# Performance work log

Hardware: AMD Instinct MI355X
Metric: run time of the kernel (lower is better)

## Reference

```python
import jax, jax.numpy as jnp
import numpy as np

N_NODES = 50000
N_EDGES = 1000000
HID = 64
L = 3
EPS_MSG = 1e-7   # GENConv message eps
EPS_SM = 1e-16   # PyG scatter-softmax denominator eps
LN_EPS = 1e-5


def layernorm(x, g, b):
    mu = jnp.mean(x, axis=-1, keepdims=True)
    var = jnp.var(x, axis=-1, keepdims=True)
    return (x - mu) * jax.lax.rsqrt(var + LN_EPS) * g + b


def genconv(x, src, dst, edge_attr, t, W1, b1, g1, be1, W2, b2):
    # message: relu(x_j + e_ij) + eps  -> [E, HID]
    msg = jax.nn.relu(x[src] + edge_attr) + EPS_MSG
    # softmax aggregation over incoming edges of each dst node
    logits = msg * t
    m = jax.ops.segment_max(logits, dst, num_segments=N_NODES)
    m = jnp.where(jnp.isfinite(m), m, 0.0)
    e = jnp.exp(logits - m[dst])
    s = jax.ops.segment_sum(e, dst, num_segments=N_NODES) + EPS_SM
    agg = jax.ops.segment_sum((e / s[dst]) * msg, dst, num_segments=N_NODES)
    # root residual + MLP [64 -> 128 -> 64]
    h = agg + x
    h = h @ W1 + b1
    h = jax.nn.relu(layernorm(h, g1, be1))
    return h @ W2 + b2


def setup_inputs() -> dict:
    key = jax.random.key(0)
    ks = jax.random.split(key, 10)
    inp = {
        'x': jax.random.normal(ks[0], (N_NODES, 16), jnp.float32),
        'edge_attr': jax.random.uniform(ks[1], (N_EDGES, 1), jnp.float32),
        'edge_index': jax.random.randint(ks[2], (2, N_EDGES), 0, N_NODES, jnp.int32),
        'W_node': jax.random.normal(ks[3], (16, HID), jnp.float32) / np.sqrt(16.0),
        'b_node': jnp.zeros((HID,), jnp.float32),
        'W_edge': jax.random.normal(ks[4], (1, HID), jnp.float32),
        'b_edge': jnp.zeros((HID,), jnp.float32),
        't': jnp.ones((L,), jnp.float32),
        'W1': jax.random.normal(ks[5], (L, HID, 2 * HID), jnp.float32) / np.sqrt(float(HID)),
        'b1': jnp.zeros((L, 2 * HID), jnp.float32),
        'ln_g': jnp.ones((L, 2 * HID), jnp.float32),
        'ln_b': jnp.zeros((L, 2 * HID), jnp.float32),
        'W2': jax.random.normal(ks[6], (L, 2 * HID, HID), jnp.float32) / np.sqrt(2.0 * HID),
        'b2': jnp.zeros((L, HID), jnp.float32),
        'norm_g': jnp.ones((L, HID), jnp.float32),
        'norm_b': jnp.zeros((L, HID), jnp.float32),
        'W_lin': jax.random.normal(ks[7], (HID, 64), jnp.float32) / np.sqrt(float(HID)),
        'b_lin': jnp.zeros((64,), jnp.float32),
    }
    return inp


def reference(x, edge_attr, edge_index, W_node, b_node, W_edge, b_edge, t,
              W1, b1, ln_g, ln_b, W2, b2, norm_g, norm_b, W_lin, b_lin):
    src, dst = edge_index[0], edge_index[1]
    h = x @ W_node + b_node                 # [N, HID]
    ea = edge_attr @ W_edge + b_edge        # [E, HID]
    # layer 0: conv only
    h = genconv(h, src, dst, ea, t[0], W1[0], b1[0], ln_g[0], ln_b[0], W2[0], b2[0])
    # layers 1..L-1: res+ blocks (norm -> relu -> conv -> residual); dropout is identity in eval
    for i in range(1, L):
        z = jax.nn.relu(layernorm(h, norm_g[i], norm_b[i]))
        h = h + genconv(z, src, dst, ea, t[i], W1[i], b1[i], ln_g[i], ln_b[i], W2[i], b2[i])
    # final norm/act reuses layer 0's norm
    h = jax.nn.relu(layernorm(h, norm_g[0], norm_b[0]))
    # adaptive avg/max pool (N, 64) -> (1, 32): pool over all nodes, channel bins of 2
    avg = h.mean(axis=0).reshape(32, 2).mean(axis=1)
    mx = h.max(axis=0).reshape(32, 2).max(axis=1)
    emb = jnp.concatenate([avg, mx])[None, :]   # [1, 64]
    return emb @ W_lin + b_lin                  # [1, 64]
```

## Files before the change

kernel.cpp:

```cpp
#include <hip/hip_runtime.h>
#include <math.h>

#define N_NODES 50000
#define N_EDGES 1000000
#define HID 64
#define SCAN_NB ((N_NODES + 1 + 255) / 256)
#define N_TILES (N_NODES / 16)
#define NB_F ((N_TILES + 3) / 4)
#define NB2 64
#define VB_S 72
#define UB_S 136
static_assert(N_NODES % 16 == 0, "tile math");
static_assert(N_NODES <= 65536, "src must fit in 16 bits");

typedef __attribute__((ext_vector_type(8))) short short8;
typedef __attribute__((ext_vector_type(4))) float f32x4;

__device__ __forceinline__ unsigned short f2bf(float x) {
    unsigned u = __float_as_uint(x);
    u += 0x7FFFu + ((u >> 16) & 1u);
    return (unsigned short)(u >> 16);
}
__device__ __forceinline__ float bfbits_hi(unsigned pk) {
    return __uint_as_float(pk & 0xFFFF0000u);
}
__device__ __forceinline__ float bf2f(unsigned short v) {
    return __uint_as_float(((unsigned)v) << 16);
}
__device__ __forceinline__ unsigned addpk(unsigned a, unsigned b) {
    float lo = __uint_as_float(a << 16) + __uint_as_float(b << 16);
    float hi = __uint_as_float(a & 0xFFFF0000u) + __uint_as_float(b & 0xFFFF0000u);
    return (unsigned)f2bf(lo) | ((unsigned)f2bf(hi) << 16);
}

__global__ __launch_bounds__(256) void k_node_encode(
    const float* __restrict__ x, const float* __restrict__ Wn,
    const float* __restrict__ bn, unsigned short* __restrict__ zb) {
    int n = blockIdx.x * 4 + (threadIdx.x >> 6);
    int c = threadIdx.x & 63;
    if (n >= N_NODES) return;
    float acc = bn[c];
    const float* xr = x + n * 16;
    #pragma unroll
    for (int k = 0; k < 16; ++k) acc = fmaf(xr[k], Wn[k * 64 + c], acc);
    zb[n * 64 + c] = f2bf(acc);
}

__global__ __launch_bounds__(256) void k_wprep(
    const float* __restrict__ W1, const float* __restrict__ W2,
    unsigned short* __restrict__ w1p, unsigned short* __restrict__ w2p) {
    int i = blockIdx.x * 256 + threadIdx.x;
    if (i >= 3 * 8192) return;
    int L = i >> 13, r = i & 8191;
    int j = r & 7, lane = (r >> 3) & 63;
    int quad = lane >> 4, col = lane & 15;
    {
        int st = r >> 9;
        int s = st >> 3, t = st & 7;
        w1p[i] = f2bf(W1[L * 8192 + (s * 32 + quad * 8 + j) * 128 + t * 16 + col]);
    }
    {
        int ft = r >> 9;
        int s = ft >> 2, t = ft & 3;
        w2p[i] = f2bf(W2[L * 8192 + (s * 32 + quad * 8 + j) * 64 + t * 16 + col]);
    }
}

__global__ __launch_bounds__(256) void k_hist_rank(const int* __restrict__ ei,
                                                   int* __restrict__ cnt, int* __restrict__ rank) {
    int i = blockIdx.x * blockDim.x + threadIdx.x;
    if (i >= N_EDGES) return;
    rank[i] = atomicAdd(&cnt[ei[N_EDGES + i]], 1);
}

__global__ __launch_bounds__(256) void k_scan1(const int* __restrict__ cnt,
                                               int* __restrict__ inc, int* __restrict__ bsum) {
    __shared__ int sh[256];
    int gi = blockIdx.x * 256 + threadIdx.x;
    int v = (gi < N_NODES + 1) ? cnt[gi] : 0;
    sh[threadIdx.x] = v;
    __syncthreads();
    #pragma unroll
    for (int d = 1; d < 256; d <<= 1) {
        int t = (threadIdx.x >= d) ? sh[threadIdx.x - d] : 0;
        __syncthreads();
        sh[threadIdx.x] += t;
        __syncthreads();
    }
    if (gi < N_NODES + 1) inc[gi] = sh[threadIdx.x];
    if (threadIdx.x == 255) bsum[blockIdx.x] = sh[255];
}

__global__ __launch_bounds__(256) void k_scan2(int* __restrict__ bsum) {
    __shared__ int sh[256];
    int t = threadIdx.x;
    sh[t] = (t < SCAN_NB) ? bsum[t] : 0;
    __syncthreads();
    #pragma unroll
    for (int d = 1; d < 256; d <<= 1) {
        int v = (t >= d) ? sh[t - d] : 0;
        __syncthreads();
        sh[t] += v;
        __syncthreads();
    }
    if (t < SCAN_NB) bsum[t] = (t == 0) ? 0 : sh[t - 1];
}

__global__ __launch_bounds__(256) void k_scan3(const int* __restrict__ inc,
                                               const int* __restrict__ cnt,
                                               const int* __restrict__ bsum,
                                               int* __restrict__ offs) {
    int gi = blockIdx.x * 256 + threadIdx.x;
    if (gi < N_NODES + 1) offs[gi] = bsum[blockIdx.x] + inc[gi] - cnt[gi];
}

__global__ __launch_bounds__(256) void k_scatter(
    const int* __restrict__ ei, const float* __restrict__ eattr,
    const int* __restrict__ offs, const int* __restrict__ rank,
    unsigned int* __restrict__ s_pack) {
    int i = blockIdx.x * blockDim.x + threadIdx.x;
    if (i >= N_EDGES) return;
    int d = ei[N_EDGES + i];
    int p = offs[d] + rank[i];
    unsigned pk = ((unsigned)f2bf(eattr[i]) << 16) | (unsigned)(ei[i] & 0xFFFF);
    s_pack[p] = pk;
}

__global__ __launch_bounds__(256) void k_agg(
    const unsigned short* __restrict__ zb, const int* __restrict__ offs,
    const unsigned int* __restrict__ s_pack,
    const float* __restrict__ We, const float* __restrict__ be,
    const float* __restrict__ t, int layer, unsigned short* __restrict__ aggb) {
    int wid = (blockIdx.x * blockDim.x + threadIdx.x) >> 6;
    int lane = threadIdx.x & 63;
    if (wid >= N_NODES) return;
    int beg = offs[wid], end = offs[wid + 1];
    float we = We[lane], bev = be[lane];
    float tl = t[layer];
    float s = 0.f, num = 0.f;
    int i = beg;
    for (; i + 7 < end; i += 8) {
        unsigned pk[8];
        #pragma unroll
        for (int j = 0; j < 8; ++j) pk[j] = s_pack[i + j];
        float zv[8];
        #pragma unroll
        for (int j = 0; j < 8; ++j) zv[j] = bf2f(zb[(pk[j] & 0xFFFFu) * 64 + lane]);
        float acc_s = 0.f, acc_n = 0.f;
        #pragma unroll
        for (int j = 0; j < 8; ++j) {
            float msg = fmaxf(zv[j] + fmaf(bfbits_hi(pk[j]), we, bev), 0.f) + 1e-7f;
            float p = __expf(msg * tl);
            acc_s += p;
            acc_n = fmaf(p, msg, acc_n);
        }
        s += acc_s;
        num += acc_n;
    }
    for (; i < end; ++i) {
        unsigned pk = s_pack[i];
        float zz = bf2f(zb[(pk & 0xFFFFu) * 64 + lane]);
        float msg = fmaxf(zz + fmaf(bfbits_hi(pk), we, bev), 0.f) + 1e-7f;
        float p = __expf(msg * tl);
        s += p;
        num = fmaf(p, msg, num);
    }
    aggb[wid * 64 + lane] = f2bf(num / (s + 1e-16f));
}

__global__ __launch_bounds__(256) void k_mlp(
    const unsigned short* __restrict__ aggb, unsigned short* __restrict__ zb,
    unsigned short* __restrict__ hb,
    const unsigned short* __restrict__ w1p, const unsigned short* __restrict__ w2p,
    const float* __restrict__ b1,
    const float* __restrict__ g1, const float* __restrict__ be1,
    const float* __restrict__ b2,
    const float* __restrict__ ng, const float* __restrict__ nb, int mode,
    float* __restrict__ pb_sum, float* __restrict__ pb_max) {
    __shared__ unsigned short vbuf[4][16 * VB_S];
    __shared__ unsigned short ubuf[4][16 * UB_S];
    __shared__ float lssum[4][4][16], lsmax[4][4][16];
    int lane = threadIdx.x & 63;
    int wave = threadIdx.x >> 6;
    int col = lane & 15, quad = lane >> 4;
    unsigned short* vb = vbuf[wave];
    unsigned short* ub = ubuf[wave];

    short8 w1f[2][8];
    #pragma unroll
    for (int s = 0; s < 2; ++s)
        #pragma unroll
        for (int t = 0; t < 8; ++t)
            w1f[s][t] = *(const short8*)&w1p[(((s * 8 + t) * 64) + lane) * 8];
    short8 w2f[4][4];
    #pragma unroll
    for (int s = 0; s < 4; ++s)
        #pragma unroll
        for (int t = 0; t < 4; ++t)
            w2f[s][t] = *(const short8*)&w2p[(((s * 4 + t) * 64) + lane) * 8];

    float b1f[8], g1f[8], e1f[8];
    #pragma unroll
    for (int t = 0; t < 8; ++t) {
        int ch = t * 16 + col;
        b1f[t] = b1[ch]; g1f[t] = g1[ch]; e1f[t] = be1[ch];
    }
    float b2f_[4], ngf[4], nbf[4];
    #pragma unroll
    for (int t = 0; t < 4; ++t) {
        b2f_[t] = b2[t * 16 + col];
        ngf[t] = ng[t * 16 + col];
        nbf[t] = nb[t * 16 + col];
    }

    float psum[4] = {0.f, 0.f, 0.f, 0.f};
    float pmax[4] = {0.f, 0.f, 0.f, 0.f};
    int nd = lane >> 2;
    int cg = (lane & 3) * 16;
    int tile = blockIdx.x * 4 + wave;

    if (tile < N_TILES) {
        int n0 = tile * 16;
        const uint4* ap = (const uint4*)(aggb + (size_t)(n0 + nd) * 64 + cg);
        const uint4* zp = (const uint4*)(zb + (size_t)(n0 + nd) * 64 + cg);
        uint4 a0 = ap[0], a1 = ap[1], z0 = zp[0], z1 = zp[1];
        uint4 r0, r1;
        r0.x = addpk(a0.x, z0.x); r0.y = addpk(a0.y, z0.y);
        r0.z = addpk(a0.z, z0.z); r0.w = addpk(a0.w, z0.w);
        r1.x = addpk(a1.x, z1.x); r1.y = addpk(a1.y, z1.y);
        r1.z = addpk(a1.z, z1.z); r1.w = addpk(a1.w, z1.w);
        uint4* vdst = (uint4*)&vb[nd * VB_S + cg];
        vdst[0] = r0;
        vdst[1] = r1;

        short8 af0 = *(const short8*)&vb[col * VB_S + quad * 8];
        short8 af1 = *(const short8*)&vb[col * VB_S + 32 + quad * 8];
        f32x4 au[8];
        #pragma unroll
        for (int t = 0; t < 8; ++t) {
            f32x4 c = {0.f, 0.f, 0.f, 0.f};
            c = __builtin_amdgcn_mfma_f32_16x16x32_bf16(af0, w1f[0][t], c, 0, 0, 0);
            c = __builtin_amdgcn_mfma_f32_16x16x32_bf16(af1, w1f[1][t], c, 0, 0, 0);
            au[t] = c;
        }
        #pragma unroll
        for (int r = 0; r < 4; ++r) {
            float sx = 0.f, sq = 0.f;
            #pragma unroll
            for (int t = 0; t < 8; ++t) {
                float v = au[t][r] + b1f[t];
                sx += v; sq += v * v;
            }
            #pragma unroll
            for (int mask = 1; mask < 16; mask <<= 1) {
                sx += __shfl_xor(sx, mask, 64);
                sq += __shfl_xor(sq, mask, 64);
            }
            float mu = sx * (1.f / 128.f);
            float var = sq * (1.f / 128.f) - mu * mu;
            float rs = rsqrtf(var + 1e-5f);
            int row = quad * 4 + r;
            #pragma unroll
            for (int t = 0; t < 8; ++t) {
                float v = au[t][r] + b1f[t];
                float y = fmaxf(fmaf((v - mu) * rs, g1f[t], e1f[t]), 0.f);
                ub[row * UB_S + t * 16 + col] = f2bf(y);
            }
        }
        f32x4 oc[4];
        #pragma unroll
        for (int t = 0; t < 4; ++t) oc[t] = (f32x4){0.f, 0.f, 0.f, 0.f};
        #pragma unroll
        for (int s = 0; s < 4; ++s) {
            short8 a = *(const short8*)&ub[col * UB_S + s * 32 + quad * 8];
            #pragma unroll
            for (int t = 0; t < 4; ++t)
                oc[t] = __builtin_amdgcn_mfma_f32_16x16x32_bf16(a, w2f[s][t], oc[t], 0, 0, 0);
        }
        #pragma unroll
        for (int r = 0; r < 4; ++r) {
            int n = n0 + quad * 4 + r;
            float val[4];
            #pragma unroll
            for (int t = 0; t < 4; ++t) {
                val[t] = oc[t][r] + b2f_[t];
                if (mode >= 1) val[t] += bf2f(hb[(size_t)n * 64 + t * 16 + col]);
            }
            if (mode <= 1) {
                #pragma unroll
                for (int t = 0; t < 4; ++t) hb[(size_t)n * 64 + t * 16 + col] = f2bf(val[t]);
            }
            float sx = 0.f, sq = 0.f;
            #pragma unroll
            for (int t = 0; t < 4; ++t) { sx += val[t]; sq += val[t] * val[t]; }
            #pragma unroll
            for (int mask = 1; mask < 16; mask <<= 1) {
                sx += __shfl_xor(sx, mask, 64);
                sq += __shfl_xor(sq, mask, 64);
            }
            float mu = sx * (1.f / 64.f);
            float var = sq * (1.f / 64.f) - mu * mu;
            float rs = rsqrtf(var + 1e-5f);
            #pragma unroll
            for (int t = 0; t < 4; ++t) {
                float y = fmaxf(fmaf((val[t] - mu) * rs, ngf[t], nbf[t]), 0.f);
                if (mode <= 1) {
                    zb[(size_t)n * 64 + t * 16 + col] = f2bf(y);
                } else {
                    psum[t] += y;
                    pmax[t] = fmaxf(pmax[t], y);
                }
            }
        }
    }
    if (mode == 2) {
        #pragma unroll
        for (int t = 0; t < 4; ++t) {
            psum[t] += __shfl_xor(psum[t], 16, 64);
            psum[t] += __shfl_xor(psum[t], 32, 64);
            pmax[t] = fmaxf(pmax[t], __shfl_xor(pmax[t], 16, 64));
            pmax[t] = fmaxf(pmax[t], __shfl_xor(pmax[t], 32, 64));
        }
        if (quad == 0) {
            #pragma unroll
            for (int t = 0; t < 4; ++t) {
                lssum[wave][t][col] = psum[t];
                lsmax[wave][t][col] = pmax[t];
            }
        }
        __syncthreads();
        if (wave == 0) {
            int t = lane >> 4, c = lane & 15;
            float s = lssum[0][t][c] + lssum[1][t][c] + lssum[2][t][c] + lssum[3][t][c];
            float mx = fmaxf(fmaxf(lsmax[0][t][c], lsmax[1][t][c]),
                             fmaxf(lsmax[2][t][c], lsmax[3][t][c]));
            pb_sum[blockIdx.x * 64 + lane] = s;
            pb_max[blockIdx.x * 64 + lane] = mx;
        }
    }
}

__global__ __launch_bounds__(256) void k_red(
    const float* __restrict__ pb_sum, const float* __restrict__ pb_max,
    float* __restrict__ p2_sum, float* __restrict__ p2_max) {
    __shared__ float sa4[4][64], sm4[4][64];
    int t = threadIdx.x;
    int ch = t & 63, part = t >> 6;
    float s = 0.f, mx = 0.f;
    for (int b = blockIdx.x + NB2 * part; b < NB_F; b += NB2 * 4) {
        s += pb_sum[b * 64 + ch];
        mx = fmaxf(mx, pb_max[b * 64 + ch]);
    }
    sa4[part][ch] = s; sm4[part][ch] = mx;
    __syncthreads();
    if (t < 64) {
        p2_sum[blockIdx.x * 64 + t] = sa4[0][t] + sa4[1][t] + sa4[2][t] + sa4[3][t];
        p2_max[blockIdx.x * 64 + t] =
            fmaxf(fmaxf(sm4[0][t], sm4[1][t]), fmaxf(sm4[2][t], sm4[3][t]));
    }
}

__global__ __launch_bounds__(256) void k_head(
    const float* __restrict__ p2_sum, const float* __restrict__ p2_max,
    const float* __restrict__ Wl, const float* __restrict__ bl, float* __restrict__ out) {
    __shared__ float sa4[4][64], sm4[4][64];
    __shared__ float sa[64], sm[64], emb[64];
    int t = threadIdx.x;
    int ch = t & 63, part = t >> 6;
    float s = 0.f, mx = 0.f;
    for (int b = part; b < NB2; b += 4) {
        s += p2_sum[b * 64 + ch];
        mx = fmaxf(mx, p2_max[b * 64 + ch]);
    }
    sa4[part][ch] = s; sm4[part][ch] = mx;
    __syncthreads();
    if (t < 64) {
        sa[t] = sa4[0][t] + sa4[1][t] + sa4[2][t] + sa4[3][t];
        sm[t] = fmaxf(fmaxf(sm4[0][t], sm4[1][t]), fmaxf(sm4[2][t], sm4[3][t]));
    }
    __syncthreads();
    if (t < 64) {
        if (t < 32) {
            emb[t] = (sa[2 * t] + sa[2 * t + 1]) * (0.5f / (float)N_NODES);
        } else {
            int i = t - 32;
            emb[t] = fmaxf(sm[2 * i], sm[2 * i + 1]);
        }
    }
    __syncthreads();
    if (t < 64) {
        float acc = bl[t];
        for (int k = 0; k < 64; ++k) acc = fmaf(emb[k], Wl[k * 64 + t], acc);
        out[t] = acc;
    }
}

extern "C" void kernel_launch(void* const* d_in, const int* in_sizes, int n_in,
                              void* d_out, int out_size, void* d_ws, size_t ws_size,
                              hipStream_t stream) {
    const float* x     = (const float*)d_in[0];
    const float* eattr = (const float*)d_in[1];
    const int*   ei    = (const int*)d_in[2];
    const float* Wn    = (const float*)d_in[3];
    const float* bn    = (const float*)d_in[4];
    const float* We    = (const float*)d_in[5];
    const float* be    = (const float*)d_in[6];
    const float* t     = (const float*)d_in[7];
    const float* W1    = (const float*)d_in[8];
    const float* b1    = (const float*)d_in[9];
    const float* lg    = (const float*)d_in[10];
    const float* lb    = (const float*)d_in[11];
    const float* W2    = (const float*)d_in[12];
    const float* b2    = (const float*)d_in[13];
    const float* ng    = (const float*)d_in[14];
    const float* nb    = (const float*)d_in[15];
    const float* Wl    = (const float*)d_in[16];
    const float* bl    = (const float*)d_in[17];
    float* out = (float*)d_out;

    char* p = (char*)d_ws;
    unsigned short* hb   = (unsigned short*)p; p += (size_t)N_NODES * 64 * 2;
    unsigned short* zb   = (unsigned short*)p; p += (size_t)N_NODES * 64 * 2;
    unsigned short* aggb = (unsigned short*)p; p += (size_t)N_NODES * 64 * 2;
    unsigned int* s_pack = (unsigned int*)p; p += (size_t)N_EDGES * 4;
    int* cnt    = (int*)p;  p += (size_t)(N_NODES + 4) * 4;
    int* offs   = (int*)p;  p += (size_t)(N_NODES + 4) * 4;
    int* inc    = (int*)p;  p += (size_t)(N_NODES + 4) * 4;
    int* bsum   = (int*)p;  p += (size_t)256 * 4;
    float* pb_sum = (float*)p; p += (size_t)NB_F * 64 * 4;
    float* pb_max = (float*)p; p += (size_t)NB_F * 64 * 4;
    float* p2_sum = (float*)p; p += (size_t)NB2 * 64 * 4;
    float* p2_max = (float*)p; p += (size_t)NB2 * 64 * 4;
    unsigned short* w1p = (unsigned short*)p; p += (size_t)3 * 8192 * 2;
    unsigned short* w2p = (unsigned short*)p; p += (size_t)3 * 8192 * 2;
    int* rank = (int*)p;    p += (size_t)N_EDGES * 4;

    hipMemsetAsync(cnt, 0, (N_NODES + 1) * sizeof(int), stream);

    k_node_encode<<<(N_NODES + 3) / 4, 256, 0, stream>>>(x, Wn, bn, zb);
    k_wprep<<<(3 * 8192 + 255) / 256, 256, 0, stream>>>(W1, W2, w1p, w2p);
    k_hist_rank<<<(N_EDGES + 255) / 256, 256, 0, stream>>>(ei, cnt, rank);
    k_scan1<<<SCAN_NB, 256, 0, stream>>>(cnt, inc, bsum);
    k_scan2<<<1, 256, 0, stream>>>(bsum);
    k_scan3<<<SCAN_NB, 256, 0, stream>>>(inc, cnt, bsum, offs);
    k_scatter<<<(N_EDGES + 255) / 256, 256, 0, stream>>>(ei, eattr, offs, rank, s_pack);

    k_agg<<<(N_NODES + 3) / 4, 256, 0, stream>>>(zb, offs, s_pack, We, be, t, 0, aggb);
    k_mlp<<<NB_F, 256, 0, stream>>>(aggb, zb, hb, w1p, w2p, b1, lg, lb, b2,
                                    ng + 64, nb + 64, 0, pb_sum, pb_max);
    k_agg<<<(N_NODES + 3) / 4, 256, 0, stream>>>(zb, offs, s_pack, We, be, t, 1, aggb);
    k_mlp<<<NB_F, 256, 0, stream>>>(aggb, zb, hb, w1p + 8192, w2p + 8192,
                                    b1 + 128, lg + 128, lb + 128, b2 + 64,
                                    ng + 128, nb + 128, 1, pb_sum, pb_max);
    k_agg<<<(N_NODES + 3) / 4, 256, 0, stream>>>(zb, offs, s_pack, We, be, t, 2, aggb);
    k_mlp<<<NB_F, 256, 0, stream>>>(aggb, zb, hb, w1p + 2 * 8192, w2p + 2 * 8192,
                                    b1 + 2 * 128, lg + 2 * 128, lb + 2 * 128, b2 + 2 * 64,
                                    ng, nb, 2, pb_sum, pb_max);

    k_red<<<NB2, 256, 0, stream>>>(pb_sum, pb_max, p2_sum, p2_max);
    k_head<<<1, 256, 0, stream>>>(p2_sum, p2_max, Wl, bl, out);
}
```

Baseline: 370.5 us.

## Stage MLP weights in LDS, use persistent blocks, coalesce h/z stores

The MLP kernel now runs a fixed grid of 512 blocks that loop over node tiles. Each block copies the packed W1/W2 bf16 weights into shared memory once, and the MFMA loops read weight fragments from LDS instead of holding 48 short8 values in registers per wave. The residual h rows are prefetched as 16-byte vectors and staged through LDS. The h and z outputs are staged the same way and written back as coalesced uint4 stores instead of scattered 2-byte stores. This cuts register pressure and global weight refetches, at the cost of more LDS traffic and a larger shared-memory footprint that may limit occupancy.

```diff
diff --git a/kernel.cpp b/kernel.cpp
--- a/kernel.cpp
+++ b/kernel.cpp
@@ -6,7 +6,7 @@
 #define HID 64
 #define SCAN_NB ((N_NODES + 1 + 255) / 256)
 #define N_TILES (N_NODES / 16)
-#define NB_F ((N_TILES + 3) / 4)
+#define NB_MLP 512
 #define NB2 64
 #define VB_S 72
 #define UB_S 136
@@ -177,6 +177,8 @@
     const float* __restrict__ b2,
     const float* __restrict__ ng, const float* __restrict__ nb, int mode,
     float* __restrict__ pb_sum, float* __restrict__ pb_max) {
+    __shared__ unsigned short w1s[8192];
+    __shared__ unsigned short w2s[8192];
     __shared__ unsigned short vbuf[4][16 * VB_S];
     __shared__ unsigned short ubuf[4][16 * UB_S];
     __shared__ float lssum[4][4][16], lsmax[4][4][16];
@@ -186,18 +188,18 @@
     unsigned short* vb = vbuf[wave];
     unsigned short* ub = ubuf[wave];
 
-    short8 w1f[2][8];
-    #pragma unroll
-    for (int s = 0; s < 2; ++s)
-        #pragma unroll
-        for (int t = 0; t < 8; ++t)
-            w1f[s][t] = *(const short8*)&w1p[(((s * 8 + t) * 64) + lane) * 8];
-    short8 w2f[4][4];
-    #pragma unroll
-    for (int s = 0; s < 4; ++s)
-        #pragma unroll
-        for (int t = 0; t < 4; ++t)
-            w2f[s][t] = *(const short8*)&w2p[(((s * 4 + t) * 64) + lane) * 8];
+    {
+        const uint4* s1 = (const uint4*)w1p;
+        const uint4* s2 = (const uint4*)w2p;
+        uint4* d1 = (uint4*)w1s;
+        uint4* d2 = (uint4*)w2s;
+        #pragma unroll
+        for (int i = 0; i < 4; ++i) {
+            d1[threadIdx.x + i * 256] = s1[threadIdx.x + i * 256];
+            d2[threadIdx.x + i * 256] = s2[threadIdx.x + i * 256];
+        }
+    }
+    __syncthreads();
 
     float b1f[8], g1f[8], e1f[8];
     #pragma unroll
@@ -217,9 +219,8 @@
     float pmax[4] = {0.f, 0.f, 0.f, 0.f};
     int nd = lane >> 2;
     int cg = (lane & 3) * 16;
-    int tile = blockIdx.x * 4 + wave;
-
-    if (tile < N_TILES) {
+
+    for (int tile = blockIdx.x * 4 + wave; tile < N_TILES; tile += NB_MLP * 4) {
         int n0 = tile * 16;
         const uint4* ap = (const uint4*)(aggb + (size_t)(n0 + nd) * 64 + cg);
         const uint4* zp = (const uint4*)(zb + (size_t)(n0 + nd) * 64 + cg);
@@ -235,12 +236,21 @@
 
         short8 af0 = *(const short8*)&vb[col * VB_S + quad * 8];
         short8 af1 = *(const short8*)&vb[col * VB_S + 32 + quad * 8];
+
+        uint4 h0, h1;
+        if (mode >= 1) {
+            const uint4* hp = (const uint4*)(hb + (size_t)(n0 + nd) * 64 + cg);
+            h0 = hp[0]; h1 = hp[1];
+        }
+
         f32x4 au[8];
         #pragma unroll
         for (int t = 0; t < 8; ++t) {
+            short8 w0 = *(const short8*)&w1s[((0 * 8 + t) * 64 + lane) * 8];
+            short8 w1 = *(const short8*)&w1s[((1 * 8 + t) * 64 + lane) * 8];
             f32x4 c = {0.f, 0.f, 0.f, 0.f};
-            c = __builtin_amdgcn_mfma_f32_16x16x32_bf16(af0, w1f[0][t], c, 0, 0, 0);
-            c = __builtin_amdgcn_mfma_f32_16x16x32_bf16(af1, w1f[1][t], c, 0, 0, 0);
+            c = __builtin_amdgcn_mfma_f32_16x16x32_bf16(af0, w0, c, 0, 0, 0);
+            c = __builtin_amdgcn_mfma_f32_16x16x32_bf16(af1, w1, c, 0, 0, 0);
             au[t] = c;
         }
         #pragma unroll
@@ -274,21 +284,24 @@
         for (int s = 0; s < 4; ++s) {
             short8 a = *(const short8*)&ub[col * UB_S + s * 32 + quad * 8];
             #pragma unroll
-            for (int t = 0; t < 4; ++t)
-                oc[t] = __builtin_amdgcn_mfma_f32_16x16x32_bf16(a, w2f[s][t], oc[t], 0, 0, 0);
+            for (int t = 0; t < 4; ++t) {
+                short8 w = *(const short8*)&w2s[((s * 4 + t) * 64 + lane) * 8];
+                oc[t] = __builtin_amdgcn_mfma_f32_16x16x32_bf16(a, w, oc[t], 0, 0, 0);
+            }
+        }
+        if (mode >= 1) {
+            uint4* hdst = (uint4*)&vb[nd * VB_S + cg];
+            hdst[0] = h0;
+            hdst[1] = h1;
         }
         #pragma unroll
         for (int r = 0; r < 4; ++r) {
-            int n = n0 + quad * 4 + r;
+            int row = quad * 4 + r;
             float val[4];
             #pragma unroll
             for (int t = 0; t < 4; ++t) {
                 val[t] = oc[t][r] + b2f_[t];
-                if (mode >= 1) val[t] += bf2f(hb[(size_t)n * 64 + t * 16 + col]);
-            }
-            if (mode <= 1) {
-                #pragma unroll
-                for (int t = 0; t < 4; ++t) hb[(size_t)n * 64 + t * 16 + col] = f2bf(val[t]);
+                if (mode >= 1) val[t] += bf2f(vb[row * VB_S + t * 16 + col]);
             }
             float sx = 0.f, sq = 0.f;
             #pragma unroll
@@ -305,12 +318,21 @@
             for (int t = 0; t < 4; ++t) {
                 float y = fmaxf(fmaf((val[t] - mu) * rs, ngf[t], nbf[t]), 0.f);
                 if (mode <= 1) {
-                    zb[(size_t)n * 64 + t * 16 + col] = f2bf(y);
+                    vb[row * VB_S + t * 16 + col] = f2bf(val[t]);
+                    ub[row * UB_S + t * 16 + col] = f2bf(y);
                 } else {
                     psum[t] += y;
                     pmax[t] = fmaxf(pmax[t], y);
                 }
             }
+        }
+        if (mode <= 1) {
+            const uint4* hsrc = (const uint4*)&vb[nd * VB_S + cg];
+            const uint4* zsrc = (const uint4*)&ub[nd * UB_S + cg];
+            uint4* hdst = (uint4*)(hb + (size_t)(n0 + nd) * 64 + cg);
+            uint4* zdst = (uint4*)(zb + (size_t)(n0 + nd) * 64 + cg);
+            hdst[0] = hsrc[0]; hdst[1] = hsrc[1];
+            zdst[0] = zsrc[0]; zdst[1] = zsrc[1];
         }
     }
     if (mode == 2) {
@@ -347,7 +369,7 @@
     int t = threadIdx.x;
     int ch = t & 63, part = t >> 6;
     float s = 0.f, mx = 0.f;
-    for (int b = blockIdx.x + NB2 * part; b < NB_F; b += NB2 * 4) {
+    for (int b = blockIdx.x + NB2 * part; b < NB_MLP; b += NB2 * 4) {
         s += pb_sum[b * 64 + ch];
         mx = fmaxf(mx, pb_max[b * 64 + ch]);
     }
@@ -427,8 +449,8 @@
     int* offs   = (int*)p;  p += (size_t)(N_NODES + 4) * 4;
     int* inc    = (int*)p;  p += (size_t)(N_NODES + 4) * 4;
     int* bsum   = (int*)p;  p += (size_t)256 * 4;
-    float* pb_sum = (float*)p; p += (size_t)NB_F * 64 * 4;
-    float* pb_max = (float*)p; p += (size_t)NB_F * 64 * 4;
+    float* pb_sum = (float*)p; p += (size_t)NB_MLP * 64 * 4;
+    float* pb_max = (float*)p; p += (size_t)NB_MLP * 64 * 4;
     float* p2_sum = (float*)p; p += (size_t)NB2 * 64 * 4;
     float* p2_max = (float*)p; p += (size_t)NB2 * 64 * 4;
     unsigned short* w1p = (unsigned short*)p; p += (size_t)3 * 8192 * 2;
@@ -446,16 +468,16 @@
     k_scatter<<<(N_EDGES + 255) / 256, 256, 0, stream>>>(ei, eattr, offs, rank, s_pack);
 
     k_agg<<<(N_NODES + 3) / 4, 256, 0, stream>>>(zb, offs, s_pack, We, be, t, 0, aggb);
-    k_mlp<<<NB_F, 256, 0, stream>>>(aggb, zb, hb, w1p, w2p, b1, lg, lb, b2,
-                                    ng + 64, nb + 64, 0, pb_sum, pb_max);
+    k_mlp<<<NB_MLP, 256, 0, stream>>>(aggb, zb, hb, w1p, w2p, b1, lg, lb, b2,
+                                      ng + 64, nb + 64, 0, pb_sum, pb_max);
     k_agg<<<(N_NODES + 3) / 4, 256, 0, stream>>>(zb, offs, s_pack, We, be, t, 1, aggb);
-    k_mlp<<<NB_F, 256, 0, stream>>>(aggb, zb, hb, w1p + 8192, w2p + 8192,
-                                    b1 + 128, lg + 128, lb + 128, b2 + 64,
-                                    ng + 128, nb + 128, 1, pb_sum, pb_max);
+    k_mlp<<<NB_MLP, 256, 0, stream>>>(aggb, zb, hb, w1p + 8192, w2p + 8192,
+                                      b1 + 128, lg + 128, lb + 128, b2 + 64,
+                                      ng + 128, nb + 128, 1, pb_sum, pb_max);
     k_agg<<<(N_NODES + 3) / 4, 256, 0, stream>>>(zb, offs, s_pack, We, be, t, 2, aggb);
-    k_mlp<<<NB_F, 256, 0, stream>>>(aggb, zb, hb, w1p + 2 * 8192, w2p + 2 * 8192,
-                                    b1 + 2 * 128, lg + 2 * 128, lb + 2 * 128, b2 + 2 * 64,
-                                    ng, nb, 2, pb_sum, pb_max);
+    k_mlp<<<NB_MLP, 256, 0, stream>>>(aggb, zb, hb, w1p + 2 * 8192, w2p + 2 * 8192,
+                                      b1 + 2 * 128, lg + 2 * 128, lb + 2 * 128, b2 + 2 * 64,
+                                      ng, nb, 2, pb_sum, pb_max);
 
     k_red<<<NB2, 256, 0, stream>>>(pb_sum, pb_max, p2_sum, p2_max);
     k_head<<<1, 256, 0, stream>>>(p2_sum, p2_max, Wl, bl, out);
```

Measured after the change: 356.2 us. 1.04x faster.
